# Performance work log

Measured on AMD Instinct MI355X. Metric: run time of the kernel, lower is better.

The kernel has to match this reference:

```python
import jax, jax.numpy as jnp
import numpy as np

N = 40000      # option nodes
E = 320000     # edges per edge type (avg in-degree 8)
NT = 3         # edge types
L = 3          # message-passing layers
D = 128        # node_dim
HID = 256      # hidden_dim
H = 4          # attention heads
C = HID // H   # per-head channels


def _ln(x, g, b):
    m = x.mean(-1, keepdims=True)
    v = ((x - m) ** 2).mean(-1, keepdims=True)
    return g * (x - m) * jax.lax.rsqrt(v + 1e-5) + b


def _gelu(x):
    return jax.nn.gelu(x, approximate=False)  # torch default = exact erf GELU


def _gat(h, src, dst, W, a_src, a_dst, bias):
    # PyG GATConv: shared src/dst linear, add_self_loops=False, eval (no dropout)
    xp = (h @ W).reshape(N, H, C)                      # (N,H,C)
    e = jax.nn.leaky_relu((xp * a_src).sum(-1)[src] + (xp * a_dst).sum(-1)[dst], 0.2)  # (E,H)
    emax = jax.ops.segment_max(e, dst, num_segments=N)
    emax = jnp.where(jnp.isfinite(emax), emax, 0.0)    # nodes with no in-edges
    ex = jnp.exp(e - emax[dst])
    den = jax.ops.segment_sum(ex, dst, num_segments=N)
    alpha = ex / (den[dst] + 1e-16)                    # segment softmax over incoming edges
    out = jax.ops.segment_sum(alpha[:, :, None] * xp[src], dst, num_segments=N)
    return out.reshape(N, HID) + bias


def _glorot(key, shape):
    fan_in = shape[-2] if len(shape) > 1 else shape[-1]
    return jax.random.normal(key, shape, jnp.float32) / np.sqrt(fan_in)


def setup_inputs() -> dict:
    key = jax.random.key(0)
    ks = jax.random.split(key, 16)
    return {
        "x": jax.random.normal(ks[0], (N, D), jnp.float32),
        "liquidity_features": jax.random.normal(ks[1], (N, 4), jnp.float32),
        "edge_index": jax.random.randint(ks[2], (NT, 2, E), 0, N, jnp.int32),
        "edge_weight": jax.random.uniform(ks[3], (NT, E), jnp.float32),
        "in_W": _glorot(ks[4], (D, HID)), "in_b": jnp.zeros((HID,)),
        "in_g": jnp.ones((HID,)), "in_bb": jnp.zeros((HID,)),
        "gat_W": _glorot(ks[5], (L, NT, HID, HID)),
        "gat_asrc": _glorot(ks[6], (L, NT, H, C)) * 0.1,
        "gat_adst": _glorot(ks[7], (L, NT, H, C)) * 0.1,
        "gat_bias": jnp.zeros((L, NT, HID)),
        "ln_g": jnp.ones((L, HID)), "ln_b": jnp.zeros((L, HID)),
        "gate_W": _glorot(ks[8], (HID + 4, 1)), "gate_b": jnp.zeros((1,)),
        "out_W1": _glorot(ks[9], (HID, HID)), "out_b1": jnp.zeros((HID,)),
        "out_g": jnp.ones((HID,)), "out_bb": jnp.zeros((HID,)),
        "out_W2": _glorot(ks[10], (HID, D)), "out_b2": jnp.zeros((D,)),
        "ro_W1": _glorot(ks[11], (D, HID)), "ro_b1": jnp.zeros((HID,)),
        "ro_W2": _glorot(ks[12], (HID, HID)), "ro_b2": jnp.zeros((HID,)),
    }


def reference(x, liquidity_features, edge_index, edge_weight, in_W, in_b, in_g, in_bb,
              gat_W, gat_asrc, gat_adst, gat_bias, ln_g, ln_b, gate_W, gate_b,
              out_W1, out_b1, out_g, out_bb, out_W2, out_b2,
              ro_W1, ro_b1, ro_W2, ro_b2):
    h = _gelu(_ln(x @ in_W + in_b, in_g, in_bb))  # input_proj
    # incoming edge-weight gate (static graph -> identical every layer)
    wsum = jnp.zeros((N,), x.dtype)
    deg = jnp.zeros((N,), x.dtype)
    for t in range(NT):
        dst = edge_index[t, 1]
        wsum = wsum.at[dst].add(edge_weight[t])
        deg = deg.at[dst].add(1.0)
    ewg = (0.5 + jax.nn.sigmoid(wsum / jnp.maximum(deg, 1.0)))[:, None]  # (N,1)
    layer_outputs = []
    for i in range(L):
        agg = jnp.zeros((N, HID), x.dtype)  # HeteroConv aggr='sum'
        for t in range(NT):
            agg = agg + _gat(h, edge_index[t, 0], edge_index[t, 1],
                             gat_W[i, t], gat_asrc[i, t], gat_adst[i, t], gat_bias[i, t])
        gate = jax.nn.sigmoid(jnp.concatenate([agg, liquidity_features], -1) @ gate_W + gate_b)
        hn = (gate * agg + (1.0 - gate) * h) * ewg   # liquidity gate + edge-weight gate
        h = _gelu(_ln(hn + h, ln_g[i], ln_b[i]))     # residual + LayerNorm + GELU
        layer_outputs.append(h)
    ho = _gelu(_ln(h @ out_W1 + out_b1, out_g, out_bb)) @ out_W2 + out_b2  # (N,D)
    surf = _gelu(ho.mean(0) @ ro_W1 + ro_b1) @ ro_W2 + ro_b2               # (HID,)
    return (ho, surf, *layer_outputs)
```

## Files before the change

### kernel.cpp

```cpp
#include <hip/hip_runtime.h>
#include <hip/hip_bf16.h>
#include <math.h>

#define NN 40000
#define EE 320000
#define NT 3
#define LL 3
#define DD 128
#define HID 256
#define NH 4
#define CC 64
#define NP 768
#define LGRID 2048

typedef __attribute__((ext_vector_type(8))) short short8;
typedef __attribute__((ext_vector_type(4))) float f32x4;

__device__ __forceinline__ float gelu_f(float x) {
    return 0.5f * x * (1.0f + erff(x * 0.70710678118654752440f));
}
__device__ __forceinline__ float lrelu_f(float x) {
    return x > 0.0f ? x : 0.2f * x;
}
__device__ __forceinline__ float bf2f(unsigned short u) {
    unsigned int x = ((unsigned int)u) << 16;
    float f;
    __builtin_memcpy(&f, &x, 4);
    return f;
}
__device__ __forceinline__ unsigned short f2bf(float f) {
    __hip_bfloat16 h = __float2bfloat16(f);
    unsigned short u;
    __builtin_memcpy(&u, &h, 2);
    return u;
}
__device__ __forceinline__ void gload16(const void* g, void* l) {
    __builtin_amdgcn_global_load_lds(
        (const __attribute__((address_space(1))) unsigned int*)g,
        (__attribute__((address_space(3))) unsigned int*)l, 16, 0, 0);
}

__global__ void wconv_k(const float* __restrict__ W, unsigned short* __restrict__ Wt,
                        int nmat, int K, int N) {
    int idx = blockIdx.x * 256 + threadIdx.x;
    int tot = nmat * K * N;
    if (idx >= tot) return;
    int m = idx / (K * N);
    int rem = idx - m * (K * N);
    int k = rem / N;
    int n = rem - k * N;
    Wt[(size_t)m * K * N + (size_t)n * K + k] = f2bf(W[idx]);
}

__global__ void xconv_k(const float* __restrict__ x, unsigned short* __restrict__ xb) {
    int idx = blockIdx.x * 256 + threadIdx.x;
    if (idx >= NN * DD / 4) return;
    float4 v = *reinterpret_cast<const float4*>(&x[(size_t)idx * 4]);
    ushort4 o;
    o.x = f2bf(v.x); o.y = f2bf(v.y); o.z = f2bf(v.z); o.w = f2bf(v.w);
    *reinterpret_cast<ushort4*>(&xb[(size_t)idx * 4]) = o;
}

__global__ __launch_bounds__(256) void gemm_mfma_k(const unsigned short* __restrict__ A,
                                                   const unsigned short* __restrict__ Bt,
                                                   const float* __restrict__ bias,
                                                   float* __restrict__ Cf,
                                                   unsigned short* __restrict__ Cb,
                                                   int M, int K, int N) {
    __shared__ __align__(16) short As[128 * 32];
    __shared__ __align__(16) short Bs[128 * 32];
    int bm = blockIdx.y * 128, bn = blockIdx.x * 128;
    int tid = threadIdx.x;
    int lane = tid & 63, w = tid >> 6;
    int wr = w >> 1, wc = w & 1;
    int l16 = lane & 15, kgrp = lane >> 4;
    f32x4 acc[4][4] = {};
    for (int k0 = 0; k0 < K; k0 += 32) {
        #pragma unroll
        for (int i = 0; i < 2; i++) {
            int chunk = (i * 4 + w) * 64 + lane;
            int row = chunk >> 2, kq = chunk & 3;
            int grow = bm + row; if (grow > M - 1) grow = M - 1;
            gload16(A + (size_t)grow * K + k0 + kq * 8, &As[(i * 4 + w) * 512]);
        }
        #pragma unroll
        for (int i = 0; i < 2; i++) {
            int chunk = (i * 4 + w) * 64 + lane;
            int row = chunk >> 2, kq = chunk & 3;
            gload16(Bt + (size_t)(bn + row) * K + k0 + kq * 8, &Bs[(i * 4 + w) * 512]);
        }
        __syncthreads();
        short8 af[4], bf[4];
        #pragma unroll
        for (int mi = 0; mi < 4; mi++) {
            int row = wr * 64 + mi * 16 + l16;
            af[mi] = *reinterpret_cast<const short8*>(&As[row * 32 + kgrp * 8]);
        }
        #pragma unroll
        for (int ni = 0; ni < 4; ni++) {
            int nrow = wc * 64 + ni * 16 + l16;
            bf[ni] = *reinterpret_cast<const short8*>(&Bs[nrow * 32 + kgrp * 8]);
        }
        #pragma unroll
        for (int mi = 0; mi < 4; mi++)
            #pragma unroll
            for (int ni = 0; ni < 4; ni++)
                acc[mi][ni] = __builtin_amdgcn_mfma_f32_16x16x32_bf16(af[mi], bf[ni], acc[mi][ni], 0, 0, 0);
        __syncthreads();
    }
    #pragma unroll
    for (int mi = 0; mi < 4; mi++) {
        #pragma unroll
        for (int r = 0; r < 4; r++) {
            int row = bm + wr * 64 + mi * 16 + (lane >> 4) * 4 + r;
            if (row < M) {
                #pragma unroll
                for (int ni = 0; ni < 4; ni++) {
                    int col = bn + wc * 64 + ni * 16 + l16;
                    float v = acc[mi][ni][r] + (bias ? bias[col] : 0.0f);
                    if (Cf) Cf[(size_t)row * N + col] = v;
                    if (Cb) Cb[(size_t)row * N + col] = f2bf(v);
                }
            }
        }
    }
}

__global__ __launch_bounds__(256) void ln_gelu_k(const float* __restrict__ y,
                                                 const float* __restrict__ g,
                                                 const float* __restrict__ b,
                                                 float* __restrict__ outf,
                                                 unsigned short* __restrict__ outb) {
    int n = blockIdx.x * 4 + (threadIdx.x >> 6);
    int lane = threadIdx.x & 63;
    float4 v = *reinterpret_cast<const float4*>(&y[(size_t)n * HID + lane * 4]);
    float s = v.x + v.y + v.z + v.w;
    float q = v.x * v.x + v.y * v.y + v.z * v.z + v.w * v.w;
    #pragma unroll
    for (int o = 32; o; o >>= 1) { s += __shfl_xor(s, o); q += __shfl_xor(q, o); }
    float mean = s * (1.0f / HID);
    float var = q * (1.0f / HID) - mean * mean;
    float rs = rsqrtf(var + 1e-5f);
    float4 gv = *reinterpret_cast<const float4*>(&g[lane * 4]);
    float4 bv = *reinterpret_cast<const float4*>(&b[lane * 4]);
    float o0 = gelu_f(gv.x * (v.x - mean) * rs + bv.x);
    float o1 = gelu_f(gv.y * (v.y - mean) * rs + bv.y);
    float o2 = gelu_f(gv.z * (v.z - mean) * rs + bv.z);
    float o3 = gelu_f(gv.w * (v.w - mean) * rs + bv.w);
    if (outf) {
        float4 ov = {o0, o1, o2, o3};
        *reinterpret_cast<float4*>(&outf[(size_t)n * HID + lane * 4]) = ov;
    }
    ushort4 ob;
    ob.x = f2bf(o0); ob.y = f2bf(o1); ob.z = f2bf(o2); ob.w = f2bf(o3);
    *reinterpret_cast<ushort4*>(&outb[(size_t)n * HID + lane * 4]) = ob;
}

__global__ void hist_k(const int* __restrict__ ei, int* __restrict__ cnt) {
    int gid = blockIdx.x * 256 + threadIdx.x;
    if (gid >= NT * EE) return;
    int t = gid / EE, e = gid - t * EE;
    int dst = ei[(size_t)t * 2 * EE + EE + e];
    atomicAdd(&cnt[t * NN + dst], 1);
}

__global__ __launch_bounds__(256) void scan1_k(const int* __restrict__ cnt, int* __restrict__ bsum, int n) {
    int i = blockIdx.x * 256 + threadIdx.x;
    int v = (i < n) ? cnt[i] : 0;
    #pragma unroll
    for (int o = 32; o; o >>= 1) v += __shfl_xor(v, o);
    __shared__ int s4[4];
    if ((threadIdx.x & 63) == 0) s4[threadIdx.x >> 6] = v;
    __syncthreads();
    if (threadIdx.x == 0) bsum[blockIdx.x] = s4[0] + s4[1] + s4[2] + s4[3];
}

__global__ __launch_bounds__(512) void scan2_k(const int* __restrict__ bsum, int* __restrict__ boff, int nb) {
    __shared__ int sh[512];
    int t = threadIdx.x;
    int v = (t < nb) ? bsum[t] : 0;
    sh[t] = v;
    __syncthreads();
    for (int o = 1; o < 512; o <<= 1) {
        int tv = (t >= o) ? sh[t - o] : 0;
        __syncthreads();
        sh[t] += tv;
        __syncthreads();
    }
    if (t < nb) boff[t] = sh[t] - v;
}

__global__ __launch_bounds__(256) void scan3_k(const int* __restrict__ cnt, const int* __restrict__ boff,
                                               int* __restrict__ roff, int n) {
    int i = blockIdx.x * 256 + threadIdx.x;
    int lane = threadIdx.x & 63, w = threadIdx.x >> 6;
    int v = (i < n) ? cnt[i] : 0;
    int s = v;
    #pragma unroll
    for (int o = 1; o < 64; o <<= 1) {
        int tv = __shfl_up(s, o);
        if (lane >= o) s += tv;
    }
    __shared__ int ws_[4];
    if (lane == 63) ws_[w] = s;
    __syncthreads();
    int add = 0;
    for (int k = 0; k < 4; k++) if (k < w) add += ws_[k];
    int incl = s + add + boff[blockIdx.x];
    if (i < n) roff[i] = incl - v;
    if (i == n - 1) roff[n] = incl;
}

__global__ void scatter_k(const int* __restrict__ ei, const float* __restrict__ ew,
                          const int* __restrict__ roff, int* __restrict__ cur,
                          int* __restrict__ csr_src, float* __restrict__ csr_ew) {
    int gid = blockIdx.x * 256 + threadIdx.x;
    if (gid >= NT * EE) return;
    int t = gid / EE, e = gid - t * EE;
    int src = ei[(size_t)t * 2 * EE + e];
    int dst = ei[(size_t)t * 2 * EE + EE + e];
    int pos = roff[t * NN + dst] + atomicAdd(&cur[t * NN + dst], 1);
    csr_src[pos] = src;
    csr_ew[pos] = ew[gid];
}

__global__ void ewg_kernel(const int* __restrict__ roff, const float* __restrict__ csr_ew,
                           float* __restrict__ ewg) {
    int n = blockIdx.x * 256 + threadIdx.x;
    if (n >= NN) return;
    float ws = 0.0f;
    int dg = 0;
    for (int t = 0; t < NT; t++) {
        int beg = roff[t * NN + n], end = roff[t * NN + n + 1];
        dg += end - beg;
        for (int e = beg; e < end; e++) ws += csr_ew[e];
    }
    float m = dg > 1 ? (float)dg : 1.0f;
    float z = ws / m;
    ewg[n] = 0.5f + 1.0f / (1.0f + __expf(-z));
}

__global__ __launch_bounds__(256) void compute_s_k(const unsigned short* __restrict__ xpa,
                                                   const float* __restrict__ asrc,
                                                   const float* __restrict__ adst,
                                                   float* __restrict__ ss,
                                                   float* __restrict__ sd) {
    int t = blockIdx.x / (NN / 4);
    int node = (blockIdx.x % (NN / 4)) * 4 + (threadIdx.x >> 6);
    int lane = threadIdx.x & 63;
    ushort4 v = *reinterpret_cast<const ushort4*>(&xpa[(size_t)node * NP + t * HID + lane * 4]);
    float4 av = *reinterpret_cast<const float4*>(&asrc[t * HID + lane * 4]);
    float4 dv = *reinterpret_cast<const float4*>(&adst[t * HID + lane * 4]);
    float x0 = bf2f(v.x), x1 = bf2f(v.y), x2 = bf2f(v.z), x3 = bf2f(v.w);
    float p = x0 * av.x + x1 * av.y + x2 * av.z + x3 * av.w;
    float q = x0 * dv.x + x1 * dv.y + x2 * dv.z + x3 * dv.w;
    #pragma unroll
    for (int o = 8; o; o >>= 1) { p += __shfl_xor(p, o); q += __shfl_xor(q, o); }
    if ((lane & 15) == 0) {
        ss[((size_t)t * NN + node) * NH + (lane >> 4)] = p;
        sd[((size_t)t * NN + node) * NH + (lane >> 4)] = q;
    }
}

__global__ __launch_bounds__(256) void layer_k(const unsigned short* __restrict__ xpa,
                                               const float* __restrict__ ss,
                                               const float* __restrict__ sd,
                                               const int* __restrict__ roff,
                                               const int* __restrict__ rsrc,
                                               const float* __restrict__ gatb,
                                               const float* __restrict__ liq,
                                               const float* __restrict__ gW,
                                               const float* __restrict__ gb,
                                               const float* __restrict__ ewg,
                                               const float* __restrict__ lg,
                                               const float* __restrict__ lb,
                                               float* __restrict__ hout,
                                               unsigned short* __restrict__ hb) {
    int wid = blockIdx.x * 4 + (threadIdx.x >> 6);
    int lane = threadIdx.x & 63;
    int h = lane >> 4;
    const int nw = LGRID * 4;
    float4 bb0 = *reinterpret_cast<const float4*>(&gatb[lane * 4]);
    float4 bb1 = *reinterpret_cast<const float4*>(&gatb[HID + lane * 4]);
    float4 bb2 = *reinterpret_cast<const float4*>(&gatb[2 * HID + lane * 4]);
    float bs0 = bb0.x + bb1.x + bb2.x;
    float bs1 = bb0.y + bb1.y + bb2.y;
    float bs2 = bb0.z + bb1.z + bb2.z;
    float bs3 = bb0.w + bb1.w + bb2.w;
    float4 gwv = *reinterpret_cast<const float4*>(&gW[lane * 4]);
    float gwl = (lane < 4) ? gW[HID + lane] : 0.0f;
    float gb0 = gb[0];
    float4 lgv = *reinterpret_cast<const float4*>(&lg[lane * 4]);
    float4 lbv = *reinterpret_cast<const float4*>(&lb[lane * 4]);

    for (int node = wid; node < NN; node += nw) {
        float agg0 = 0, agg1 = 0, agg2 = 0, agg3 = 0;
        #pragma unroll
        for (int t = 0; t < NT; t++) {
            int base = t * NN;
            int beg = roff[base + node], end = roff[base + node + 1];
            if (beg == end) continue;
            float sdh = sd[(size_t)(base + node) * NH + h];
            float den = 0, a0 = 0, a1 = 0, a2 = 0, a3 = 0;
            int sp = rsrc[beg];
            float svp = ss[(size_t)(base + sp) * NH + h];
            ushort4 xrp = *reinterpret_cast<const ushort4*>(&xpa[(size_t)sp * NP + t * HID + lane * 4]);
            for (int e = beg; e < end; e++) {
                float sv_c = svp;
                ushort4 xr_c = xrp;
                int en = (e + 1 < end) ? (e + 1) : e;
                int sn = rsrc[en];
                svp = ss[(size_t)(base + sn) * NH + h];
                xrp = *reinterpret_cast<const ushort4*>(&xpa[(size_t)sn * NP + t * HID + lane * 4]);
                float wg = __expf(lrelu_f(sv_c + sdh));
                den += wg;
                a0 += wg * bf2f(xr_c.x);
                a1 += wg * bf2f(xr_c.y);
                a2 += wg * bf2f(xr_c.z);
                a3 += wg * bf2f(xr_c.w);
            }
            float inv = 1.0f / (den + 1e-16f);
            agg0 += a0 * inv; agg1 += a1 * inv; agg2 += a2 * inv; agg3 += a3 * inv;
        }
        agg0 += bs0; agg1 += bs1; agg2 += bs2; agg3 += bs3;
        float part = agg0 * gwv.x + agg1 * gwv.y + agg2 * gwv.z + agg3 * gwv.w;
        if (lane < 4) part += liq[node * 4 + lane] * gwl;
        #pragma unroll
        for (int o = 32; o; o >>= 1) part += __shfl_xor(part, o);
        float gate = 1.0f / (1.0f + __expf(-(part + gb0)));
        float eg = ewg[node];
        ushort4 hu = *reinterpret_cast<const ushort4*>(&hb[(size_t)node * HID + lane * 4]);
        float h0 = bf2f(hu.x), h1 = bf2f(hu.y), h2 = bf2f(hu.z), h3 = bf2f(hu.w);
        float v0 = (gate * agg0 + (1.0f - gate) * h0) * eg + h0;
        float v1 = (gate * agg1 + (1.0f - gate) * h1) * eg + h1;
        float v2 = (gate * agg2 + (1.0f - gate) * h2) * eg + h2;
        float v3 = (gate * agg3 + (1.0f - gate) * h3) * eg + h3;
        float s = v0 + v1 + v2 + v3;
        float q = v0 * v0 + v1 * v1 + v2 * v2 + v3 * v3;
        #pragma unroll
        for (int o = 32; o; o >>= 1) { s += __shfl_xor(s, o); q += __shfl_xor(q, o); }
        float mean = s * (1.0f / HID);
        float var = q * (1.0f / HID) - mean * mean;
        float rs = rsqrtf(var + 1e-5f);
        float o0 = gelu_f(lgv.x * (v0 - mean) * rs + lbv.x);
        float o1 = gelu_f(lgv.y * (v1 - mean) * rs + lbv.y);
        float o2 = gelu_f(lgv.z * (v2 - mean) * rs + lbv.z);
        float o3 = gelu_f(lgv.w * (v3 - mean) * rs + lbv.w);
        float4 ov = {o0, o1, o2, o3};
        *reinterpret_cast<float4*>(&hout[(size_t)node * HID + lane * 4]) = ov;
        ushort4 ob;
        ob.x = f2bf(o0); ob.y = f2bf(o1); ob.z = f2bf(o2); ob.w = f2bf(o3);
        *reinterpret_cast<ushort4*>(&hb[(size_t)node * HID + lane * 4]) = ob;
    }
}

__global__ __launch_bounds__(128) void colpart_k(const float* __restrict__ ho,
                                                 float* __restrict__ part) {
    int c = threadIdx.x, b = blockIdx.x;
    float s = 0.0f;
    for (int r = b; r < NN; r += 256) s += ho[(size_t)r * DD + c];
    part[b * DD + c] = s;
}

__global__ __launch_bounds__(256) void readout_k(const float* __restrict__ part,
                                                 const float* __restrict__ W1,
                                                 const float* __restrict__ b1,
                                                 const float* __restrict__ W2,
                                                 const float* __restrict__ b2,
                                                 float* __restrict__ surf) {
    __shared__ float m[DD];
    __shared__ float a1[HID];
    int t = threadIdx.x;
    if (t < DD) {
        float s = 0.0f;
        for (int b = 0; b < 256; b++) s += part[b * DD + t];
        m[t] = s / (float)NN;
    }
    __syncthreads();
    float s1 = b1[t];
    for (int k = 0; k < DD; k++) s1 += m[k] * W1[k * HID + t];
    a1[t] = gelu_f(s1);
    __syncthreads();
    float s2 = b2[t];
    for (int k = 0; k < HID; k++) s2 += a1[k] * W2[k * HID + t];
    surf[t] = s2;
}

extern "C" void kernel_launch(void* const* d_in, const int* in_sizes, int n_in,
                              void* d_out, int out_size, void* d_ws, size_t ws_size,
                              hipStream_t stream) {
    const float* x       = (const float*)d_in[0];
    const float* liq     = (const float*)d_in[1];
    const int*   ei      = (const int*)d_in[2];
    const float* ew      = (const float*)d_in[3];
    const float* in_W    = (const float*)d_in[4];
    const float* in_b    = (const float*)d_in[5];
    const float* in_g    = (const float*)d_in[6];
    const float* in_bb   = (const float*)d_in[7];
    const float* gat_W   = (const float*)d_in[8];
    const float* gat_as  = (const float*)d_in[9];
    const float* gat_ad  = (const float*)d_in[10];
    const float* gat_b   = (const float*)d_in[11];
    const float* ln_g    = (const float*)d_in[12];
    const float* ln_b    = (const float*)d_in[13];
    const float* gate_W  = (const float*)d_in[14];
    const float* gate_b  = (const float*)d_in[15];
    const float* out_W1  = (const float*)d_in[16];
    const float* out_b1  = (const float*)d_in[17];
    const float* out_g   = (const float*)d_in[18];
    const float* out_bb  = (const float*)d_in[19];
    const float* out_W2  = (const float*)d_in[20];
    const float* out_b2  = (const float*)d_in[21];
    const float* ro_W1   = (const float*)d_in[22];
    const float* ro_b1   = (const float*)d_in[23];
    const float* ro_W2   = (const float*)d_in[24];
    const float* ro_b2   = (const float*)d_in[25];

    float* out = (float*)d_out;
    float* out_ho   = out;
    float* out_surf = out + (size_t)NN * DD;
    float* out_h[3];
    out_h[0] = out_surf + HID;
    out_h[1] = out_h[0] + (size_t)NN * HID;
    out_h[2] = out_h[1] + (size_t)NN * HID;

    char* wsb = (char*)d_ws;
    size_t off = 0;
    auto alloc = [&](size_t bytes) { char* p = wsb + off; off += (bytes + 255) & ~(size_t)255; return p; };
    unsigned short* xpa = (unsigned short*)alloc((size_t)NN * NP * 2);
    float* Cf32 = (float*)xpa;
    unsigned short* xb = xpa + (size_t)NN * 512;
    unsigned short* hb = (unsigned short*)alloc((size_t)NN * HID * 2);
    unsigned short* Wt_in  = (unsigned short*)alloc((size_t)DD * HID * 2);
    unsigned short* Wt_gat = (unsigned short*)alloc((size_t)LL * NT * HID * HID * 2);
    unsigned short* Wt_o1  = (unsigned short*)alloc((size_t)HID * HID * 2);
    unsigned short* Wt_o2  = (unsigned short*)alloc((size_t)HID * DD * 2);
    size_t cew_b = (size_t)NT * EE * 4;
    size_t cnt_b = (size_t)NT * NN * 4;
    char* R = alloc(cew_b + cnt_b + 2 * 2048 * 4);
    float* cew = (float*)R;
    int* cnt   = (int*)(R + cew_b);
    int* bsum  = (int*)(R + cew_b + cnt_b);
    int* boff  = bsum + 2048;
    float* ss  = (float*)R;
    float* sd  = ss + (size_t)NT * NN * NH;
    int* roff  = (int*)alloc(((size_t)NT * NN + 1) * 4);
    int* rsrc  = (int*)alloc((size_t)NT * EE * 4);
    float* ewg = (float*)alloc((size_t)NN * 4);
    float* cpart = (float*)alloc((size_t)256 * DD * 4);

    const int NSC = (NT * NN + 255) / 256;

    wconv_k<<<(DD * HID + 255) / 256, 256, 0, stream>>>(in_W, Wt_in, 1, DD, HID);
    wconv_k<<<(LL * NT * HID * HID + 255) / 256, 256, 0, stream>>>(gat_W, Wt_gat, LL * NT, HID, HID);
    wconv_k<<<(HID * HID + 255) / 256, 256, 0, stream>>>(out_W1, Wt_o1, 1, HID, HID);
    wconv_k<<<(HID * DD + 255) / 256, 256, 0, stream>>>(out_W2, Wt_o2, 1, HID, DD);
    xconv_k<<<(NN * DD / 4 + 255) / 256, 256, 0, stream>>>(x, xb);

    gemm_mfma_k<<<dim3(HID / 128, (NN + 127) / 128), 256, 0, stream>>>(
        xb, Wt_in, in_b, Cf32, nullptr, NN, DD, HID);
    ln_gelu_k<<<NN / 4, 256, 0, stream>>>(Cf32, in_g, in_bb, nullptr, hb);

    hipMemsetAsync(cnt, 0, cnt_b, stream);
    hist_k<<<(NT * EE + 255) / 256, 256, 0, stream>>>(ei, cnt);
    scan1_k<<<NSC, 256, 0, stream>>>(cnt, bsum, NT * NN);
    scan2_k<<<1, 512, 0, stream>>>(bsum, boff, NSC);
    scan3_k<<<NSC, 256, 0, stream>>>(cnt, boff, roff, NT * NN);
    hipMemsetAsync(cnt, 0, cnt_b, stream);
    scatter_k<<<(NT * EE + 255) / 256, 256, 0, stream>>>(ei, ew, roff, cnt, rsrc, cew);
    ewg_kernel<<<(NN + 255) / 256, 256, 0, stream>>>(roff, cew, ewg);

    for (int i = 0; i < LL; i++) {
        gemm_mfma_k<<<dim3(NP / 128, (NN + 127) / 128), 256, 0, stream>>>(
            hb, Wt_gat + (size_t)i * NP * HID, nullptr, nullptr, xpa, NN, HID, NP);
        compute_s_k<<<NT * (NN / 4), 256, 0, stream>>>(
            xpa, gat_as + (size_t)i * NT * HID, gat_ad + (size_t)i * NT * HID, ss, sd);
        layer_k<<<LGRID, 256, 0, stream>>>(
            xpa, ss, sd, roff, rsrc, gat_b + (size_t)i * NT * HID,
            liq, gate_W, gate_b, ewg, ln_g + i * HID, ln_b + i * HID,
            out_h[i], hb);
    }

    gemm_mfma_k<<<dim3(HID / 128, (NN + 127) / 128), 256, 0, stream>>>(
        hb, Wt_o1, out_b1, Cf32, nullptr, NN, HID, HID);
    ln_gelu_k<<<NN / 4, 256, 0, stream>>>(Cf32, out_g, out_bb, nullptr, hb);
    gemm_mfma_k<<<dim3(DD / 128, (NN + 127) / 128), 256, 0, stream>>>(
        hb, Wt_o2, out_b2, out_ho, nullptr, NN, HID, DD);

    colpart_k<<<256, 128, 0, stream>>>(out_ho, cpart);
    readout_k<<<1, 256, 0, stream>>>(cpart, ro_W1, ro_b1, ro_W2, ro_b2, out_surf);
}
```

Measured before the change: 838.6 us.

## Store GAT projections in FP8 e4m3 and remap GEMM tiles across XCDs

```diff
diff --git a/kernel.cpp b/kernel.cpp
--- a/kernel.cpp
+++ b/kernel.cpp
@@ -1,5 +1,6 @@
 #include <hip/hip_runtime.h>
 #include <hip/hip_bf16.h>
+#include <hip/hip_fp8.h>
 #include <math.h>
 
 #define NN 40000
@@ -34,6 +35,15 @@
     __builtin_memcpy(&u, &h, 2);
     return u;
 }
+__device__ __forceinline__ float fp8tof(unsigned char b) {
+    __hip_fp8_e4m3 q;
+    q.__x = (__hip_fp8_storage_t)b;
+    return (float)q;
+}
+__device__ __forceinline__ unsigned char ftofp8(float f) {
+    __hip_fp8_e4m3 q(f);
+    return (unsigned char)q.__x;
+}
 __device__ __forceinline__ void gload16(const void* g, void* l) {
     __builtin_amdgcn_global_load_lds(
         (const __attribute__((address_space(1))) unsigned int*)g,
@@ -66,10 +76,18 @@
                                                    const float* __restrict__ bias,
                                                    float* __restrict__ Cf,
                                                    unsigned short* __restrict__ Cb,
+                                                   unsigned char* __restrict__ Cq,
                                                    int M, int K, int N) {
     __shared__ __align__(16) short As[128 * 32];
     __shared__ __align__(16) short Bs[128 * 32];
-    int bm = blockIdx.y * 128, bn = blockIdx.x * 128;
+    int gdx = gridDim.x;
+    int nwg = gdx * gridDim.y;
+    int f = blockIdx.y * gdx + blockIdx.x;
+    int q8 = nwg >> 3, r8 = nwg & 7;
+    int xcd = f & 7, idx8 = f >> 3;
+    int nf = (xcd < r8 ? xcd * (q8 + 1) : r8 * (q8 + 1) + (xcd - r8) * q8) + idx8;
+    int bn = (nf % gdx) * 128;
+    int bm = (nf / gdx) * 128;
     int tid = threadIdx.x;
     int lane = tid & 63, w = tid >> 6;
     int wr = w >> 1, wc = w & 1;
@@ -120,6 +138,7 @@
                     float v = acc[mi][ni][r] + (bias ? bias[col] : 0.0f);
                     if (Cf) Cf[(size_t)row * N + col] = v;
                     if (Cb) Cb[(size_t)row * N + col] = f2bf(v);
+                    if (Cq) Cq[(size_t)row * N + col] = ftofp8(v);
                 }
             }
         }
@@ -240,7 +259,7 @@
     ewg[n] = 0.5f + 1.0f / (1.0f + __expf(-z));
 }
 
-__global__ __launch_bounds__(256) void compute_s_k(const unsigned short* __restrict__ xpa,
+__global__ __launch_bounds__(256) void compute_s_k(const unsigned char* __restrict__ xpa8,
                                                    const float* __restrict__ asrc,
                                                    const float* __restrict__ adst,
                                                    float* __restrict__ ss,
@@ -248,10 +267,10 @@
     int t = blockIdx.x / (NN / 4);
     int node = (blockIdx.x % (NN / 4)) * 4 + (threadIdx.x >> 6);
     int lane = threadIdx.x & 63;
-    ushort4 v = *reinterpret_cast<const ushort4*>(&xpa[(size_t)node * NP + t * HID + lane * 4]);
+    uchar4 v = *reinterpret_cast<const uchar4*>(&xpa8[(size_t)node * NP + t * HID + lane * 4]);
     float4 av = *reinterpret_cast<const float4*>(&asrc[t * HID + lane * 4]);
     float4 dv = *reinterpret_cast<const float4*>(&adst[t * HID + lane * 4]);
-    float x0 = bf2f(v.x), x1 = bf2f(v.y), x2 = bf2f(v.z), x3 = bf2f(v.w);
+    float x0 = fp8tof(v.x), x1 = fp8tof(v.y), x2 = fp8tof(v.z), x3 = fp8tof(v.w);
     float p = x0 * av.x + x1 * av.y + x2 * av.z + x3 * av.w;
     float q = x0 * dv.x + x1 * dv.y + x2 * dv.z + x3 * dv.w;
     #pragma unroll
@@ -262,7 +281,7 @@
     }
 }
 
-__global__ __launch_bounds__(256) void layer_k(const unsigned short* __restrict__ xpa,
+__global__ __launch_bounds__(256) void layer_k(const unsigned char* __restrict__ xpa8,
                                                const float* __restrict__ ss,
                                                const float* __restrict__ sd,
                                                const int* __restrict__ roff,
@@ -304,20 +323,20 @@
             float den = 0, a0 = 0, a1 = 0, a2 = 0, a3 = 0;
             int sp = rsrc[beg];
             float svp = ss[(size_t)(base + sp) * NH + h];
-            ushort4 xrp = *reinterpret_cast<const ushort4*>(&xpa[(size_t)sp * NP + t * HID + lane * 4]);
+            uchar4 xrp = *reinterpret_cast<const uchar4*>(&xpa8[(size_t)sp * NP + t * HID + lane * 4]);
             for (int e = beg; e < end; e++) {
                 float sv_c = svp;
-                ushort4 xr_c = xrp;
+                uchar4 xr_c = xrp;
                 int en = (e + 1 < end) ? (e + 1) : e;
                 int sn = rsrc[en];
                 svp = ss[(size_t)(base + sn) * NH + h];
-                xrp = *reinterpret_cast<const ushort4*>(&xpa[(size_t)sn * NP + t * HID + lane * 4]);
+                xrp = *reinterpret_cast<const uchar4*>(&xpa8[(size_t)sn * NP + t * HID + lane * 4]);
                 float wg = __expf(lrelu_f(sv_c + sdh));
                 den += wg;
-                a0 += wg * bf2f(xr_c.x);
-                a1 += wg * bf2f(xr_c.y);
-                a2 += wg * bf2f(xr_c.z);
-                a3 += wg * bf2f(xr_c.w);
+                a0 += wg * fp8tof(xr_c.x);
+                a1 += wg * fp8tof(xr_c.y);
+                a2 += wg * fp8tof(xr_c.z);
+                a3 += wg * fp8tof(xr_c.w);
             }
             float inv = 1.0f / (den + 1e-16f);
             agg0 += a0 * inv; agg1 += a1 * inv; agg2 += a2 * inv; agg3 += a3 * inv;
@@ -427,9 +446,10 @@
     char* wsb = (char*)d_ws;
     size_t off = 0;
     auto alloc = [&](size_t bytes) { char* p = wsb + off; off += (bytes + 255) & ~(size_t)255; return p; };
-    unsigned short* xpa = (unsigned short*)alloc((size_t)NN * NP * 2);
-    float* Cf32 = (float*)xpa;
-    unsigned short* xb = xpa + (size_t)NN * 512;
+    char* big = alloc((size_t)NN * HID * 4 + (size_t)NN * DD * 2);
+    float* Cf32 = (float*)big;
+    unsigned char* xpa8 = (unsigned char*)big;
+    unsigned short* xb = (unsigned short*)(big + (size_t)NN * HID * 4);
     unsigned short* hb = (unsigned short*)alloc((size_t)NN * HID * 2);
     unsigned short* Wt_in  = (unsigned short*)alloc((size_t)DD * HID * 2);
     unsigned short* Wt_gat = (unsigned short*)alloc((size_t)LL * NT * HID * HID * 2);
@@ -458,7 +478,7 @@
     xconv_k<<<(NN * DD / 4 + 255) / 256, 256, 0, stream>>>(x, xb);
 
     gemm_mfma_k<<<dim3(HID / 128, (NN + 127) / 128), 256, 0, stream>>>(
-        xb, Wt_in, in_b, Cf32, nullptr, NN, DD, HID);
+        xb, Wt_in, in_b, Cf32, nullptr, nullptr, NN, DD, HID);
     ln_gelu_k<<<NN / 4, 256, 0, stream>>>(Cf32, in_g, in_bb, nullptr, hb);
 
     hipMemsetAsync(cnt, 0, cnt_b, stream);
@@ -472,20 +492,20 @@
 
     for (int i = 0; i < LL; i++) {
         gemm_mfma_k<<<dim3(NP / 128, (NN + 127) / 128), 256, 0, stream>>>(
-            hb, Wt_gat + (size_t)i * NP * HID, nullptr, nullptr, xpa, NN, HID, NP);
+            hb, Wt_gat + (size_t)i * NP * HID, nullptr, nullptr, nullptr, xpa8, NN, HID, NP);
         compute_s_k<<<NT * (NN / 4), 256, 0, stream>>>(
-            xpa, gat_as + (size_t)i * NT * HID, gat_ad + (size_t)i * NT * HID, ss, sd);
+            xpa8, gat_as + (size_t)i * NT * HID, gat_ad + (size_t)i * NT * HID, ss, sd);
         layer_k<<<LGRID, 256, 0, stream>>>(
-            xpa, ss, sd, roff, rsrc, gat_b + (size_t)i * NT * HID,
+            xpa8, ss, sd, roff, rsrc, gat_b + (size_t)i * NT * HID,
             liq, gate_W, gate_b, ewg, ln_g + i * HID, ln_b + i * HID,
             out_h[i], hb);
     }
 
     gemm_mfma_k<<<dim3(HID / 128, (NN + 127) / 128), 256, 0, stream>>>(
-        hb, Wt_o1, out_b1, Cf32, nullptr, NN, HID, HID);
+        hb, Wt_o1, out_b1, Cf32, nullptr, nullptr, NN, HID, HID);
     ln_gelu_k<<<NN / 4, 256, 0, stream>>>(Cf32, out_g, out_bb, nullptr, hb);
     gemm_mfma_k<<<dim3(DD / 128, (NN + 127) / 128), 256, 0, stream>>>(
-        hb, Wt_o2, out_b2, out_ho, nullptr, NN, HID, DD);
+        hb, Wt_o2, out_b2, out_ho, nullptr, nullptr, NN, HID, DD);
 
     colpart_k<<<256, 128, 0, stream>>>(out_ho, cpart);
     readout_k<<<1, 256, 0, stream>>>(cpart, ro_W1, ro_b1, ro_W2, ro_b2, out_surf);
```

After: 825.2 us. Within noise of the previous version (-1.6%).

## Remap GEMM tiles across XCDs and batch four edge gathers per iteration

Applied to the files above, without the earlier changes.

```diff
diff --git a/kernel.cpp b/kernel.cpp
--- a/kernel.cpp
+++ b/kernel.cpp
@@ -69,7 +69,14 @@
                                                    int M, int K, int N) {
     __shared__ __align__(16) short As[128 * 32];
     __shared__ __align__(16) short Bs[128 * 32];
-    int bm = blockIdx.y * 128, bn = blockIdx.x * 128;
+    int gdx = gridDim.x;
+    int nwg = gdx * gridDim.y;
+    int f = blockIdx.y * gdx + blockIdx.x;
+    int q8 = nwg >> 3, r8 = nwg & 7;
+    int xcd = f & 7, idx8 = f >> 3;
+    int nf = (xcd < r8 ? xcd * (q8 + 1) : r8 * (q8 + 1) + (xcd - r8) * q8) + idx8;
+    int bn = (nf % gdx) * 128;
+    int bm = (nf / gdx) * 128;
     int tid = threadIdx.x;
     int lane = tid & 63, w = tid >> 6;
     int wr = w >> 1, wc = w & 1;
@@ -302,22 +309,29 @@
             if (beg == end) continue;
             float sdh = sd[(size_t)(base + node) * NH + h];
             float den = 0, a0 = 0, a1 = 0, a2 = 0, a3 = 0;
-            int sp = rsrc[beg];
-            float svp = ss[(size_t)(base + sp) * NH + h];
-            ushort4 xrp = *reinterpret_cast<const ushort4*>(&xpa[(size_t)sp * NP + t * HID + lane * 4]);
-            for (int e = beg; e < end; e++) {
-                float sv_c = svp;
-                ushort4 xr_c = xrp;
-                int en = (e + 1 < end) ? (e + 1) : e;
-                int sn = rsrc[en];
-                svp = ss[(size_t)(base + sn) * NH + h];
-                xrp = *reinterpret_cast<const ushort4*>(&xpa[(size_t)sn * NP + t * HID + lane * 4]);
-                float wg = __expf(lrelu_f(sv_c + sdh));
-                den += wg;
-                a0 += wg * bf2f(xr_c.x);
-                a1 += wg * bf2f(xr_c.y);
-                a2 += wg * bf2f(xr_c.z);
-                a3 += wg * bf2f(xr_c.w);
+            int last = end - 1;
+            for (int e = beg; e < end; e += 4) {
+                int e1 = e + 1 > last ? last : e + 1;
+                int e2 = e + 2 > last ? last : e + 2;
+                int e3 = e + 3 > last ? last : e + 3;
+                int s0 = rsrc[e], s1 = rsrc[e1], s2 = rsrc[e2], s3 = rsrc[e3];
+                float sv0 = ss[(size_t)(base + s0) * NH + h];
+                float sv1 = ss[(size_t)(base + s1) * NH + h];
+                float sv2 = ss[(size_t)(base + s2) * NH + h];
+                float sv3 = ss[(size_t)(base + s3) * NH + h];
+                ushort4 x0 = *reinterpret_cast<const ushort4*>(&xpa[(size_t)s0 * NP + t * HID + lane * 4]);
+                ushort4 x1 = *reinterpret_cast<const ushort4*>(&xpa[(size_t)s1 * NP + t * HID + lane * 4]);
+                ushort4 x2 = *reinterpret_cast<const ushort4*>(&xpa[(size_t)s2 * NP + t * HID + lane * 4]);
+                ushort4 x3 = *reinterpret_cast<const ushort4*>(&xpa[(size_t)s3 * NP + t * HID + lane * 4]);
+                float w0 = __expf(lrelu_f(sv0 + sdh));
+                float w1 = (e + 1 <= last) ? __expf(lrelu_f(sv1 + sdh)) : 0.0f;
+                float w2 = (e + 2 <= last) ? __expf(lrelu_f(sv2 + sdh)) : 0.0f;
+                float w3 = (e + 3 <= last) ? __expf(lrelu_f(sv3 + sdh)) : 0.0f;
+                den += (w0 + w1) + (w2 + w3);
+                a0 += w0 * bf2f(x0.x) + w1 * bf2f(x1.x) + w2 * bf2f(x2.x) + w3 * bf2f(x3.x);
+                a1 += w0 * bf2f(x0.y) + w1 * bf2f(x1.y) + w2 * bf2f(x2.y) + w3 * bf2f(x3.y);
+                a2 += w0 * bf2f(x0.z) + w1 * bf2f(x1.z) + w2 * bf2f(x2.z) + w3 * bf2f(x3.z);
+                a3 += w0 * bf2f(x0.w) + w1 * bf2f(x1.w) + w2 * bf2f(x2.w) + w3 * bf2f(x3.w);
             }
             float inv = 1.0f / (den + 1e-16f);
             agg0 += a0 * inv; agg1 += a1 * inv; agg2 += a2 * inv; agg3 += a3 * inv;
```

Measured after the change: 814.3 us. -2.9%, faster.
